# Kernel tuning notes

Hardware: AMD Instinct MI355X
Metric: run time of the kernel (lower is better)

The kernel has to match this reference:

```python
import jax, jax.numpy as jnp
import numpy as np

ALPHA = 0.2
NEG = -9e15


def _gru(x, Wih, Whh, bih, bhh):
    # x: [B, T, F]; PyTorch nn.GRU cell equations, scan over time.
    H = Whh.shape[1]
    xg = jnp.einsum('btf,gf->btg', x, Wih) + bih  # [B,T,3H]

    def step(h, gi):
        gh = h @ Whh.T + bhh
        ir, iz, inn = jnp.split(gi, 3, axis=-1)
        hr, hz, hn = jnp.split(gh, 3, axis=-1)
        r = jax.nn.sigmoid(ir + hr)
        z = jax.nn.sigmoid(iz + hz)
        n = jnp.tanh(inn + r * hn)
        h = (1.0 - z) * n + z * h
        return h, h

    h0 = jnp.zeros((x.shape[0], H), x.dtype)
    _, ys = jax.lax.scan(step, h0, jnp.swapaxes(xg, 0, 1))
    return jnp.swapaxes(ys, 0, 1)  # [B,T,H]


def _gru_attn(x, Wih, Whh, bih, bhh, aw, ab):
    out = _gru(x, Wih, Whh, bih, bhh)              # [B,T,H]
    w = jax.nn.softmax(out @ aw + ab, axis=1)       # [B,T,1]
    return jnp.sum(out * w, axis=1)                 # [B,H]


def _gat(h, mask, W, a):
    # GraphAttentionLayer with concat=True: elu(softmax(mask(leakyrelu(Wh1+Wh2^T))) @ Wh)
    Wh = h @ W                                      # [N,O]
    O = W.shape[1]
    e = jax.nn.leaky_relu((Wh @ a[:O]) + (Wh @ a[O:]).T, ALPHA)  # [N,N]
    att = jax.nn.softmax(jnp.where(mask, e, NEG), axis=1)
    return jax.nn.elu(att @ Wh)


def setup_inputs() -> dict:
    key = jax.random.key(0)
    ks = iter(jax.random.split(key, 40))
    B, S, Wk, D, F = 1, 2048, 32, 5, 16
    H, E, NS = 128, 128, 16

    def rn(shape, scale=0.1):
        return jax.random.normal(next(ks), shape, jnp.float32) * scale

    inp = {
        'stock_features': jax.random.normal(next(ks), (B, S, Wk, D, F), jnp.float32),
        'stock_to_sector': jax.random.randint(next(ks), (S,), 0, NS, jnp.int32),
        'inter_adj': jax.random.randint(next(ks), (NS, NS), 0, 2, jnp.int32),
        'gru1_Wih': rn((3 * H, F)), 'gru1_Whh': rn((3 * H, H)),
        'gru1_bih': rn((3 * H,)), 'gru1_bhh': rn((3 * H,)),
        'attn1_w': rn((H, 1)), 'attn1_b': rn((1,)),
        'gat_intra_W': rn((H, E)), 'gat_intra_a': rn((2 * E, 1)),
        'grug_Wih': rn((3 * E, E)), 'grug_Whh': rn((3 * E, E)),
        'grug_bih': rn((3 * E,)), 'grug_bhh': rn((3 * E,)),
        'attng_w': rn((E, 1)), 'attng_b': rn((1,)),
        'grua_Wih': rn((3 * E, H)), 'grua_Whh': rn((3 * E, E)),
        'grua_bih': rn((3 * E,)), 'grua_bhh': rn((3 * E,)),
        'attna_w': rn((E, 1)), 'attna_b': rn((1,)),
        'gat_inter_W': rn((E, E)), 'gat_inter_a': rn((2 * E, 1)),
        'fusion_w': rn((3 * E, E)), 'fusion_b': rn((E,)),
        'ret_w': rn((E, 1)), 'ret_b': rn((1,)),
        'mov_w': rn((E, 1)), 'mov_b': rn((1,)),
    }
    return inp


def reference(stock_features, stock_to_sector, inter_adj,
              gru1_Wih, gru1_Whh, gru1_bih, gru1_bhh, attn1_w, attn1_b,
              gat_intra_W, gat_intra_a,
              grug_Wih, grug_Whh, grug_bih, grug_bhh, attng_w, attng_b,
              grua_Wih, grua_Whh, grua_bih, grua_bhh, attna_w, attna_b,
              gat_inter_W, gat_inter_a,
              fusion_w, fusion_b, ret_w, ret_b, mov_w, mov_b):
    B, S, Wk, D, F = stock_features.shape
    H = gru1_Whh.shape[1]
    E = gat_intra_W.shape[1]
    NS = inter_adj.shape[0]

    # Short-term: GRU-attention over days, vectorized over (batch, stock, week).
    x = stock_features.reshape(B * S * Wk, D, F)
    short = _gru_attn(x, gru1_Wih, gru1_Whh, gru1_bih, gru1_bhh, attn1_w, attn1_b)
    short = short.reshape(B, S, Wk, H)

    # Intra-sector GAT on last-week embeddings; per-sector softmax == block mask.
    same_sector = stock_to_sector[:, None] == stock_to_sector[None, :]  # [S,S]
    last = short[:, :, -1, :]                                            # [B,S,H]
    intra = jax.vmap(lambda h: _gat(h, same_sector, gat_intra_W, gat_intra_a))(last)  # [B,S,E]

    # Long-term GRU-attentions.
    lg = _gru_attn(intra.reshape(B * S, 1, E), grug_Wih, grug_Whh, grug_bih, grug_bhh,
                   attng_w, attng_b).reshape(B, S, E)
    la = _gru_attn(short.reshape(B * S, Wk, H), grua_Wih, grua_Whh, grua_bih, grua_bhh,
                   attna_w, attna_b).reshape(B, S, E)

    # Sector embeddings = mean of stock long-term embeddings per sector.
    def sector_mean(g):
        sums = jax.ops.segment_sum(g, stock_to_sector, num_segments=NS)
        cnt = jax.ops.segment_sum(jnp.ones((g.shape[0], 1), g.dtype),
                                  stock_to_sector, num_segments=NS)
        return sums / jnp.maximum(cnt, 1.0)

    sec = jax.vmap(sector_mean)(lg)                                      # [B,NS,E]
    imask = inter_adj > 0
    sec_out = jax.vmap(lambda h: _gat(h, imask, gat_inter_W, gat_inter_a))(sec)
    sec_ps = sec_out[:, stock_to_sector, :]                               # [B,S,E]

    fused = jnp.concatenate([lg, la, sec_ps], axis=-1) @ fusion_w + fusion_b
    returns = (fused @ ret_w + ret_b)[..., 0]
    moves = jax.nn.sigmoid(fused @ mov_w + mov_b)[..., 0]
    return jnp.stack([returns, moves])  # [2,B,S]
```

## Files before the change

kernel.cpp:

```cpp
#include <hip/hip_runtime.h>
#include <math.h>

#define LRELU_A 0.2f
#define NEGBIG (-9.0e15f)

typedef _Float16 f16;
typedef _Float16 f16x8 __attribute__((ext_vector_type(8)));
typedef _Float16 f16x4 __attribute__((ext_vector_type(4)));
typedef float floatx4 __attribute__((ext_vector_type(4)));

__device__ __forceinline__ float rcpf(float x){ return __builtin_amdgcn_rcpf(x); }
__device__ __forceinline__ float sigm(float x){ return rcpf(1.0f+__expf(-x)); }
__device__ __forceinline__ float gru_fuse(float xr, float xz, float xn_pre, float ghn, float h){
    float Er = __expf(-xr);
    float r  = rcpf(1.0f + Er);
    float En = __expf(2.0f*(xn_pre + r*ghn));
    float Ez = __expf(-xz);
    float Dn = En + 1.0f;
    float num = fmaf(h, Dn, (En - 1.0f)*Ez);
    float den = Dn * (1.0f + Ez);
    return num * rcpf(den);
}
__device__ __forceinline__ f16x8 load_cvt8(const float* __restrict__ p){
    float4 a = *(const float4*)p; float4 b = *(const float4*)(p+4);
    f16x8 r; r[0]=(f16)a.x; r[1]=(f16)a.y; r[2]=(f16)a.z; r[3]=(f16)a.w;
    r[4]=(f16)b.x; r[5]=(f16)b.y; r[6]=(f16)b.z; r[7]=(f16)b.w;
    return r;
}
#define MFMA16(A,B,C) __builtin_amdgcn_mfma_f32_16x16x32_f16((A),(B),(C),0,0,0)

__global__ __launch_bounds__(256) void prep_kernel(
    const float* __restrict__ g1Wih, const float* __restrict__ g1Whh,
    const float* __restrict__ gaWih, const float* __restrict__ gaWhh,
    const float* __restrict__ giW,   const float* __restrict__ fw,
    const int* __restrict__ sec,
    f16* __restrict__ Wcat1, f16* __restrict__ WcatA,
    f16* __restrict__ WT, f16* __restrict__ fwT,
    int* __restrict__ memflat, int* __restrict__ pos,
    int* __restrict__ cnt, int* __restrict__ base)
{
    __shared__ int cs[16], wsc[16];
    const int b = blockIdx.x, tid = threadIdx.x;
    if (b < 160){
        for (int idx = b*256+tid; idx < 512*160; idx += 160*256){
            int r = idx/160, k = idx - r*160;
            float v = 0.0f;
            if (r < 256){ if (k < 32){ if (k < 16) v = g1Wih[r*16+k]; } else v = g1Whh[r*128 + (k-32)]; }
            else if (r < 384){ if (k < 16) v = g1Wih[r*16+k]; }
            else { if (k >= 32) v = g1Whh[(r-128)*128 + (k-32)]; }
            Wcat1[idx] = (f16)v;
        }
    } else if (b < 416){
        for (int idx = (b-160)*256+tid; idx < 512*256; idx += 256*256){
            int r = idx >> 8, k = idx & 255;
            float v = 0.0f;
            if (r < 256){ v = (k < 128) ? gaWih[r*128+k] : gaWhh[r*128 + (k-128)]; }
            else if (r < 384){ if (k < 128) v = gaWih[r*128+k]; }
            else { if (k >= 128) v = gaWhh[(r-128)*128 + (k-128)]; }
            WcatA[idx] = (f16)v;
        }
    } else if (b < 480){
        int idx = (b-416)*256+tid;
        int r = idx >> 7, c = idx & 127;
        WT[c*128 + r] = (f16)giW[idx];
    } else if (b < 672){
        int idx = (b-480)*256+tid;
        int r = idx >> 7, c = idx & 127;
        fwT[c*384 + r] = (f16)fw[idx];
    } else {
        if (tid < 16) cs[tid] = 0;
        __syncthreads();
        for (int s = tid; s < 2048; s += 256) atomicAdd(&cs[sec[s]], 1);
        __syncthreads();
        if (tid == 0){
            int acc = 0;
            for (int g=0; g<16; g++){ cnt[g]=cs[g]; base[g]=acc; wsc[g]=acc; acc+=cs[g]; }
        }
        __syncthreads();
        for (int s = tid; s < 2048; s += 256){
            int g = sec[s];
            int p = atomicAdd(&wsc[g], 1);
            memflat[p] = s;
            pos[s] = p;
        }
    }
}

__global__ __launch_bounds__(512,2) void gru_short(
    const float* __restrict__ x, const f16* __restrict__ Wcat,
    const float* __restrict__ bih, const float* __restrict__ bhh,
    const float* __restrict__ aw, const float* __restrict__ ab,
    f16* __restrict__ out)
{
    __shared__ __align__(16) f16 xs[5][32][40];
    __shared__ __align__(16) f16 hs[2][32][136];
    __shared__ float scpart[2][8][32];
    const int tid = threadIdx.x, w = tid>>6, lane = tid&63;
    const int c = lane&15, quad = lane>>4;

    { f16x4 z4 = {0,0,0,0};
      f16x4* zx = (f16x4*)&xs[0][0][0];
      for (int i=tid; i<1600; i+=512) zx[i] = z4; }

    const int jrow = w*16 + c;
    f16x8 Ar[5], Az[5], Agi, Agh[4];
#pragma unroll
    for (int kb=0;kb<5;kb++){
        Ar[kb] = *(const f16x8*)&Wcat[(size_t)(jrow)*160 + kb*32 + quad*8];
        Az[kb] = *(const f16x8*)&Wcat[(size_t)(128+jrow)*160 + kb*32 + quad*8];
    }
    Agi = *(const f16x8*)&Wcat[(size_t)(256+jrow)*160 + quad*8];
#pragma unroll
    for (int i=0;i<4;i++)
        Agh[i] = *(const f16x8*)&Wcat[(size_t)(384+jrow)*160 + 32 + i*32 + quad*8];

    float brz_r[4], brz_z[4], b_in[4], b_hn[4], awr[4];
#pragma unroll
    for (int r=0;r<4;r++){
        int j = w*16 + quad*4 + r;
        brz_r[r] = bih[j] + bhh[j];
        brz_z[r] = bih[128+j] + bhh[128+j];
        b_in[r] = bih[256+j]; b_hn[r] = bhh[256+j];
        awr[r] = aw[j];
    }
    const float abv = ab[0];

#pragma unroll 1
    for (int tile=0; tile<4; ++tile){
        const int s0 = (blockIdx.x*4 + tile)*32;
        { f16x4 z4 = {0,0,0,0};
          f16x4* zh = (f16x4*)&hs[1][0][0];
          for (int i=tid; i<1088; i+=512) zh[i] = z4; }
        for (int i=tid; i<640; i+=512){
            int s = i/20, q = i - 20*s;
            float4 v = *(const float4*)&x[(size_t)(s0+s)*80 + q*4];
            int t = (q*4)>>4, f = (q*4)&15;
            f16x4 h4; h4[0]=(f16)v.x; h4[1]=(f16)v.y; h4[2]=(f16)v.z; h4[3]=(f16)v.w;
            *(f16x4*)&xs[t][s][f] = h4;
        }
        float hreg[2][4], aacc[2][4], l_[2] = {0.0f, 0.0f};
#pragma unroll
        for (int st=0; st<2; st++)
#pragma unroll
            for (int r=0;r<4;r++){ hreg[st][r]=0.0f; aacc[st][r]=0.0f; }
        __syncthreads();

#pragma unroll 1
        for (int t=0; t<5; ++t){
            const int rp = (t&1)^1, wp = t&1;
            f16x8 Bx[2], Bh[2][4];
#pragma unroll
            for (int st=0; st<2; st++){
                Bx[st] = *(const f16x8*)&xs[t][st*16+c][quad*8];
#pragma unroll
                for (int i=0;i<4;i++)
                    Bh[st][i] = *(const f16x8*)&hs[rp][st*16+c][i*32+quad*8];
            }
            if (t > 0){
#pragma unroll
                for (int st=0; st<2; st++){
                    float sc = abv;
#pragma unroll
                    for (int ww=0; ww<8; ww++) sc += scpart[rp][ww][st*16+c];
                    float e = __expf(sc);
                    l_[st] += e;
#pragma unroll
                    for (int r=0;r<4;r++) aacc[st][r] += e*hreg[st][r];
                }
            }
            float sp[2];
#pragma unroll
            for (int st=0; st<2; st++){
                floatx4 ar = {0,0,0,0}, az = {0,0,0,0}, agi = {0,0,0,0}, agh = {0,0,0,0};
                ar = MFMA16(Ar[0], Bx[st], ar);
                az = MFMA16(Az[0], Bx[st], az);
                agi = MFMA16(Agi, Bx[st], agi);
#pragma unroll
                for (int i=0;i<4;i++){
                    ar = MFMA16(Ar[1+i], Bh[st][i], ar);
                    az = MFMA16(Az[1+i], Bh[st][i], az);
                    agh = MFMA16(Agh[i], Bh[st][i], agh);
                }
                f16x4 h4;
                sp[st] = 0.0f;
#pragma unroll
                for (int r=0;r<4;r++){
                    float hn = gru_fuse(ar[r] + brz_r[r], az[r] + brz_z[r],
                                        agi[r] + b_in[r], agh[r] + b_hn[r], hreg[st][r]);
                    hreg[st][r] = hn; h4[r] = (f16)hn;
                    sp[st] += hn * awr[r];
                }
                *(f16x4*)&hs[wp][st*16 + c][w*16 + quad*4] = h4;
            }
#pragma unroll
            for (int st=0; st<2; st++){
                sp[st] += __shfl_xor(sp[st], 16);
                sp[st] += __shfl_xor(sp[st], 32);
            }
            if (lane < 16){ scpart[wp][w][lane] = sp[0]; scpart[wp][w][16+lane] = sp[1]; }
            __syncthreads();
        }
#pragma unroll
        for (int st=0; st<2; st++){
            float sc = abv;
#pragma unroll
            for (int ww=0; ww<8; ww++) sc += scpart[0][ww][st*16+c];
            float e = __expf(sc);
            l_[st] += e;
            float inv = rcpf(l_[st]);
            f16x4 h4;
#pragma unroll
            for (int r=0;r<4;r++) h4[r] = (f16)((aacc[st][r] + e*hreg[st][r])*inv);
            *(f16x4*)&hs[0][st*16 + c][w*16 + quad*4] = h4;
        }
        __syncthreads();
        { int s = tid>>4, p = tid&15;
          *(f16x8*)&out[(size_t)(s0+s)*128 + p*8] = *(const f16x8*)&hs[0][s][p*8]; }
    }
}

__global__ __launch_bounds__(512,2) void gru_la_gatprep(
    const f16* __restrict__ xseq, const f16* __restrict__ Wcat,
    const float* __restrict__ bih, const float* __restrict__ bhh,
    const float* __restrict__ aw, const float* __restrict__ ab,
    f16* __restrict__ out,
    const f16* __restrict__ WT, const float* __restrict__ gia,
    const int* __restrict__ memflat,
    f16* __restrict__ Whs, float* __restrict__ ers, float* __restrict__ el)
{
    __shared__ __align__(16) f16 xs[2][16][136];
    __shared__ __align__(16) f16 hs[2][16][136];
    __shared__ float scpart[2][8][16];
    __shared__ __align__(16) float tbuf[32][132];
    __shared__ int rows[32];
    const int tid = threadIdx.x, w = tid>>6, lane = tid&63;
    const int c = lane&15, quad = lane>>4;

    if (blockIdx.x >= 256){
        const int p0 = (blockIdx.x-256)*32;
        if (tid < 32) rows[tid] = memflat[p0 + tid];
        __syncthreads();
        f16x8 A[2][4];
#pragma unroll
        for (int mt=0;mt<2;mt++)
#pragma unroll
            for (int kb=0;kb<4;kb++)
                A[mt][kb] = *(const f16x8*)&xseq[((size_t)rows[mt*16+c]*32 + 31)*128 + kb*32 + quad*8];
        {
            int jb = w;
            f16x8 B[4];
#pragma unroll
            for (int kb=0;kb<4;kb++)
                B[kb] = *(const f16x8*)&WT[(size_t)(jb*16+c)*128 + kb*32 + quad*8];
            floatx4 acc[2] = {{0,0,0,0},{0,0,0,0}};
#pragma unroll
            for (int kb=0;kb<4;kb++){
                acc[0] = MFMA16(A[0][kb], B[kb], acc[0]);
                acc[1] = MFMA16(A[1][kb], B[kb], acc[1]);
            }
#pragma unroll
            for (int mt=0;mt<2;mt++)
#pragma unroll
                for (int r=0;r<4;r++)
                    tbuf[mt*16 + quad*4 + r][jb*16 + c] = acc[mt][r];
        }
        __syncthreads();
        for (int i=tid; i<1024; i+=512){
            int s = i>>5, p = i&31;
            float4 v = *(const float4*)&tbuf[s][p*4];
            f16x4 h4; h4[0]=(f16)v.x; h4[1]=(f16)v.y; h4[2]=(f16)v.z; h4[3]=(f16)v.w;
            *(f16x4*)&Whs[(size_t)(p0+s)*128 + p*4] = h4;
        }
        for (int k=0; k<4; k++){
            int row = w*4 + k;
            float w0 = tbuf[row][lane], w1 = tbuf[row][64+lane];
            float v1 = w0*gia[lane]     + w1*gia[64+lane];
            float v2 = w0*gia[128+lane] + w1*gia[192+lane];
#pragma unroll
            for (int off=32; off; off>>=1){ v1 += __shfl_down(v1,off); v2 += __shfl_down(v2,off); }
            if (lane==0){ el[rows[row]] = v1; ers[p0+row] = v2; }
        }
        return;
    }
    const int s0 = blockIdx.x*8;
    { f16x4 z4 = {0,0,0,0};
      f16x4* za = (f16x4*)&xs[0][0][0];
      for (int i=tid; i<1088; i+=512) za[i] = z4;
      f16x4* zh = (f16x4*)&hs[0][0][0];
      for (int i=tid; i<1088; i+=512) zh[i] = z4; }
    __syncthreads();
    if (tid < 128){
        int s = tid>>4, p = tid&15;
        *(f16x8*)&xs[0][s][p*8] = *(const f16x8*)&xseq[((size_t)(s0+s)*32 + 0)*128 + p*8];
    }
    const int jrow = w*16 + c;
    f16x8 Ar[8], Az[8], Agi[4], Agh[4];
#pragma unroll
    for (int kb=0;kb<8;kb++){
        Ar[kb] = *(const f16x8*)&Wcat[(size_t)(jrow)*256 + kb*32 + quad*8];
        Az[kb] = *(const f16x8*)&Wcat[(size_t)(128+jrow)*256 + kb*32 + quad*8];
    }
#pragma unroll
    for (int i=0;i<4;i++){
        Agi[i] = *(const f16x8*)&Wcat[(size_t)(256+jrow)*256 + i*32 + quad*8];
        Agh[i] = *(const f16x8*)&Wcat[(size_t)(384+jrow)*256 + 128 + i*32 + quad*8];
    }
    float brz_r[4], brz_z[4], b_in[4], b_hn[4], awr[4];
#pragma unroll
    for (int r=0;r<4;r++){
        int j = w*16 + quad*4 + r;
        brz_r[r] = bih[j] + bhh[j];
        brz_z[r] = bih[128+j] + bhh[128+j];
        b_in[r] = bih[256+j]; b_hn[r] = bhh[256+j];
        awr[r] = aw[j];
    }
    const float abv = ab[0];
    float hreg[4] = {0,0,0,0}, aacc[4] = {0,0,0,0}, l_ = 0.0f;
    __syncthreads();

#pragma unroll 1
    for (int t=0; t<32; ++t){
        const int rp = (t&1)^1, wp = t&1, xp = t&1;
        f16x8 Bx[4], Bh[4];
#pragma unroll
        for (int i=0;i<4;i++){
            Bx[i] = *(const f16x8*)&xs[xp][c][i*32+quad*8];
            Bh[i] = *(const f16x8*)&hs[rp][c][i*32+quad*8];
        }
        f16x8 xstage;
        const bool do_stage = (t < 31) && (tid < 128);
        if (do_stage){
            int s = tid>>4, p = tid&15;
            xstage = *(const f16x8*)&xseq[((size_t)(s0+s)*32 + t+1)*128 + p*8];
        }
        if (t > 0){
            float sc = abv;
#pragma unroll
            for (int ww=0; ww<8; ww++) sc += scpart[rp][ww][c];
            float e = __expf(sc);
            l_ += e;
#pragma unroll
            for (int r=0;r<4;r++) aacc[r] += e*hreg[r];
        }
        floatx4 ar = {0,0,0,0}, az = {0,0,0,0}, agi = {0,0,0,0}, agh = {0,0,0,0};
#pragma unroll
        for (int i=0;i<4;i++){
            ar = MFMA16(Ar[i], Bx[i], ar);
            az = MFMA16(Az[i], Bx[i], az);
            agi = MFMA16(Agi[i], Bx[i], agi);
        }
#pragma unroll
        for (int i=0;i<4;i++){
            ar = MFMA16(Ar[4+i], Bh[i], ar);
            az = MFMA16(Az[4+i], Bh[i], az);
            agh = MFMA16(Agh[i], Bh[i], agh);
        }
        f16x4 h4;
        float sp = 0.0f;
#pragma unroll
        for (int r=0;r<4;r++){
            float hn = gru_fuse(ar[r] + brz_r[r], az[r] + brz_z[r],
                                agi[r] + b_in[r], agh[r] + b_hn[r], hreg[r]);
            hreg[r] = hn; h4[r] = (f16)hn;
            sp += hn * awr[r];
        }
        *(f16x4*)&hs[wp][c][w*16 + quad*4] = h4;
        if (do_stage){
            int s = tid>>4, p = tid&15;
            *(f16x8*)&xs[xp^1][s][p*8] = xstage;
        }
        sp += __shfl_xor(sp, 16);
        sp += __shfl_xor(sp, 32);
        if (lane < 16) scpart[wp][w][lane] = sp;
        __syncthreads();
    }
    {
        float sc = abv;
#pragma unroll
        for (int ww=0; ww<8; ww++) sc += scpart[1][ww][c];
        float e = __expf(sc);
        l_ += e;
        float inv = rcpf(l_);
        f16x4 h4;
#pragma unroll
        for (int r=0;r<4;r++) h4[r] = (f16)((aacc[r] + e*hreg[r])*inv);
        *(f16x4*)&hs[1][c][w*16 + quad*4] = h4;
    }
    __syncthreads();
    if (tid < 128){
        int s = tid>>4, p = tid&15;
        *(f16x8*)&out[(size_t)(s0+s)*128 + p*8] = *(const f16x8*)&hs[1][s][p*8];
    }
}

__global__ __launch_bounds__(256) void gat_intra_mem_kernel(
    const f16* __restrict__ Whs, const float* __restrict__ ers,
    const float* __restrict__ el, const int* __restrict__ sec,
    const int* __restrict__ cnt, const int* __restrict__ base,
    f16* __restrict__ outp, int S)
{
    int wave = threadIdx.x>>6, lane = threadIdx.x&63;
    int i = blockIdx.x*4 + wave;
    if (i>=S) return;
    int g = sec[i];
    int n = cnt[g], b = base[g];
    float eli = el[i];
    float m = -INFINITY;
    for (int jj=lane; jj<n; jj+=64){
        float v = eli + ers[b+jj]; v = v>0.f? v : LRELU_A*v;
        m = fmaxf(m, v);
    }
#pragma unroll
    for (int off=32; off; off>>=1) m = fmaxf(m, __shfl_xor(m, off));
    float l = 0.f, c0=0.f, c1=0.f;
#pragma unroll 4
    for (int jj=0; jj<n; jj++){
        float v = eli + ers[b+jj]; v = v>0.f? v : LRELU_A*v;
        float p = __expf(v-m);
        l += p;
        c0 += p*(float)Whs[(size_t)(b+jj)*128 + lane];
        c1 += p*(float)Whs[(size_t)(b+jj)*128 + 64 + lane];
    }
    float il = rcpf(l);
    c0 *= il; c1 *= il;
    outp[(size_t)i*128+lane]    = (f16)(c0>0.f? c0 : expm1f(c0));
    outp[(size_t)i*128+64+lane] = (f16)(c1>0.f? c1 : expm1f(c1));
}

__global__ __launch_bounds__(256) void lg_mfma(
    const f16* __restrict__ intra16, const float* __restrict__ Wih,
    const float* __restrict__ bih, const float* __restrict__ bhh,
    const int* __restrict__ pos,
    f16* __restrict__ lgout, f16* __restrict__ lgs)
{
    __shared__ __align__(16) f16 tbuf[32][136];
    const int tid = threadIdx.x, w = tid>>6, lane = tid&63;
    const int c = lane&15, quad = lane>>4;
    const int s0 = blockIdx.x*32;
    f16x8 A[2][4];
#pragma unroll
    for (int mt=0;mt<2;mt++)
#pragma unroll
        for (int kb=0;kb<4;kb++)
            A[mt][kb] = *(const f16x8*)&intra16[(size_t)(s0+mt*16+c)*128 + kb*32 + quad*8];
#pragma unroll
    for (int i=0;i<2;i++){
        int jb = w*2 + i;
        int j = jb*16 + c;
        f16x8 Br[4], Bz[4], Bn[4];
#pragma unroll
        for (int kb=0;kb<4;kb++){
            Br[kb] = load_cvt8(&Wih[(size_t)(j)*128 + kb*32 + quad*8]);
            Bz[kb] = load_cvt8(&Wih[(size_t)(128+j)*128 + kb*32 + quad*8]);
            Bn[kb] = load_cvt8(&Wih[(size_t)(256+j)*128 + kb*32 + quad*8]);
        }
        float b_r = bih[j] + bhh[j];
        float b_z = bih[128+j] + bhh[128+j];
        float b_i = bih[256+j], b_h = bhh[256+j];
        floatx4 ar[2] = {{0,0,0,0},{0,0,0,0}};
        floatx4 az[2] = {{0,0,0,0},{0,0,0,0}};
        floatx4 an[2] = {{0,0,0,0},{0,0,0,0}};
#pragma unroll
        for (int kb=0;kb<4;kb++)
#pragma unroll
            for (int mt=0;mt<2;mt++){
                ar[mt] = MFMA16(A[mt][kb], Br[kb], ar[mt]);
                az[mt] = MFMA16(A[mt][kb], Bz[kb], az[mt]);
                an[mt] = MFMA16(A[mt][kb], Bn[kb], an[mt]);
            }
#pragma unroll
        for (int mt=0;mt<2;mt++)
#pragma unroll
            for (int r=0;r<4;r++){
                float Er = __expf(-(ar[mt][r] + b_r));
                float rg = rcpf(1.0f + Er);
                float En = __expf(2.0f*(an[mt][r] + b_i + rg*b_h));
                float Ez = __expf(-(az[mt][r] + b_z));
                float v = (En - 1.0f)*Ez * rcpf((En + 1.0f)*(1.0f + Ez));
                tbuf[mt*16 + quad*4 + r][j] = (f16)v;
            }
    }
    __syncthreads();
    for (int i=tid; i<512; i+=256){
        int s = i>>4, p = i&15;
        f16x8 v = *(const f16x8*)&tbuf[s][p*8];
        *(f16x8*)&lgout[(size_t)(s0+s)*128 + p*8] = v;
        *(f16x8*)&lgs[(size_t)pos[s0+s]*128 + p*8] = v;
    }
}

__global__ __launch_bounds__(1024) void gat_inter_fused(
    const f16* __restrict__ lgs, const int* __restrict__ cnt,
    const int* __restrict__ base, const int* __restrict__ adj,
    const float* __restrict__ W, const float* __restrict__ a,
    float* __restrict__ outp)
{
    __shared__ __align__(16) float hs[16][132];
    __shared__ __align__(16) float Whs[16][132];
    __shared__ float el[16], er[16];
    __shared__ float att[16][16];
    const int tid = threadIdx.x, w = tid>>6, lane = tid&63;

    {
        int n = cnt[w], b = base[w];
        const int rowoff = lane>>4;
        const int colb = (lane&15)*8;
        float acc[8] = {0,0,0,0,0,0,0,0};
        for (int r = rowoff; r < n; r += 4){
            f16x8 v = *(const f16x8*)&lgs[(size_t)(b+r)*128 + colb];
#pragma unroll
            for (int k=0;k<8;k++) acc[k] += (float)v[k];
        }
#pragma unroll
        for (int k=0;k<8;k++){
            acc[k] += __shfl_xor(acc[k], 16);
            acc[k] += __shfl_xor(acc[k], 32);
        }
        if (lane < 16){
            float inv = rcpf(fmaxf((float)n, 1.0f));
#pragma unroll
            for (int k=0;k<8;k++) hs[w][colb+k] = acc[k]*inv;
        }
    }
    __syncthreads();
#pragma unroll
    for (int i=0;i<2;i++){
        int idx = i*1024 + tid; int o = idx&127, s = idx>>7;
        float a0=0.f,a1=0.f,a2=0.f,a3=0.f;
        for (int j=0;j<128;j+=4){
            a0 += hs[s][j]  *W[(j  )*128+o];
            a1 += hs[s][j+1]*W[(j+1)*128+o];
            a2 += hs[s][j+2]*W[(j+2)*128+o];
            a3 += hs[s][j+3]*W[(j+3)*128+o];
        }
        Whs[s][o]=(a0+a1)+(a2+a3);
    }
    __syncthreads();
    {
        int half = lane>>5, l = lane&31;
        const float* av = a + half*128;
        float acc2 = 0.f;
#pragma unroll
        for (int k=0;k<4;k++) acc2 += Whs[w][l+32*k]*av[l+32*k];
#pragma unroll
        for (int off=1; off<32; off<<=1) acc2 += __shfl_xor(acc2, off);
        if (l==0){ if (half) er[w]=acc2; else el[w]=acc2; }
    }
    __syncthreads();
    if (tid<16){
        int i=tid; float m=NEGBIG; float e[16];
        for(int j=0;j<16;j++){
            float v = el[i]+er[j]; v = v>0.f? v : LRELU_A*v;
            e[j] = (adj[i*16+j]>0)? v : NEGBIG;
            m = fmaxf(m,e[j]);
        }
        float l=0.f;
        for(int j=0;j<16;j++){ float p=__expf(e[j]-m); att[i][j]=p; l+=p; }
        float il = rcpf(l);
        for(int j=0;j<16;j++) att[i][j] *= il;
    }
    __syncthreads();
#pragma unroll
    for (int i=0;i<2;i++){
        int idx=i*1024+tid; int o=idx&127, s=idx>>7;
        float acc=0.f;
#pragma unroll
        for(int j=0;j<16;j++) acc += att[s][j]*Whs[j][o];
        outp[s*128+o] = acc>0.f? acc : expm1f(acc);
    }
}

__global__ __launch_bounds__(256) void fused_mfma(
    const f16* __restrict__ lg16, const f16* __restrict__ la16,
    const float* __restrict__ seco, const int* __restrict__ sec,
    const f16* __restrict__ fwT,
    const float* __restrict__ fb, const float* __restrict__ rw,
    const float* __restrict__ rb, const float* __restrict__ mw,
    const float* __restrict__ mb, float* __restrict__ outp)
{
    __shared__ float rpart[4][32], mpart[4][32];
    const int tid = threadIdx.x, w = tid>>6, lane = tid&63;
    const int c = lane&15, quad = lane>>4;
    const int s0 = blockIdx.x*32;
    f16x8 A[2][12];
#pragma unroll
    for (int mt=0;mt<2;mt++){
        int row = s0 + mt*16 + c;
        int g = sec[row];
#pragma unroll
        for (int kb=0;kb<4;kb++){
            A[mt][kb]   = *(const f16x8*)&lg16[(size_t)row*128 + kb*32 + quad*8];
            A[mt][4+kb] = *(const f16x8*)&la16[(size_t)row*128 + kb*32 + quad*8];
            A[mt][8+kb] = load_cvt8(&seco[(size_t)g*128 + kb*32 + quad*8]);
        }
    }
    float rsum[2][4] = {{0,0,0,0},{0,0,0,0}};
    float msum[2][4] = {{0,0,0,0},{0,0,0,0}};
#pragma unroll
    for (int i=0;i<2;i++){
        int jb = w*2 + i;
        int col = jb*16 + c;
        f16x8 B[12];
#pragma unroll
        for (int kb=0;kb<12;kb++)
            B[kb] = *(const f16x8*)&fwT[(size_t)col*384 + kb*32 + quad*8];
        floatx4 acc[2] = {{0,0,0,0},{0,0,0,0}};
#pragma unroll
        for (int kb=0;kb<12;kb++){
            acc[0] = MFMA16(A[0][kb], B[kb], acc[0]);
            acc[1] = MFMA16(A[1][kb], B[kb], acc[1]);
        }
        float fbv = fb[col], rwv = rw[col], mwv = mw[col];
#pragma unroll
        for (int mt=0;mt<2;mt++)
#pragma unroll
            for (int r=0;r<4;r++){
                float fu = acc[mt][r] + fbv;
                rsum[mt][r] += fu*rwv;
                msum[mt][r] += fu*mwv;
            }
    }
#pragma unroll
    for (int mt=0;mt<2;mt++)
#pragma unroll
        for (int r=0;r<4;r++){
#pragma unroll
            for (int off=1; off<16; off<<=1){
                rsum[mt][r] += __shfl_xor(rsum[mt][r], off);
                msum[mt][r] += __shfl_xor(msum[mt][r], off);
            }
            if (c==0){
                rpart[w][mt*16 + quad*4 + r] = rsum[mt][r];
                mpart[w][mt*16 + quad*4 + r] = msum[mt][r];
            }
        }
    __syncthreads();
    if (tid < 32){
        int s = tid;
        float rs = rb[0], ms = mb[0];
#pragma unroll
        for (int ww=0; ww<4; ww++){ rs += rpart[ww][s]; ms += mpart[ww][s]; }
        outp[s0+s] = rs;
        outp[2048 + s0 + s] = sigm(ms);
    }
}

extern "C" void kernel_launch(void* const* d_in, const int* in_sizes, int n_in,
                              void* d_out, int out_size, void* d_ws, size_t ws_size,
                              hipStream_t stream) {
    const float* sf    = (const float*)d_in[0];
    const int*   sec   = (const int*)  d_in[1];
    const int*   adj   = (const int*)  d_in[2];
    const float* g1Wih = (const float*)d_in[3];
    const float* g1Whh = (const float*)d_in[4];
    const float* g1bih = (const float*)d_in[5];
    const float* g1bhh = (const float*)d_in[6];
    const float* a1w   = (const float*)d_in[7];
    const float* a1b   = (const float*)d_in[8];
    const float* giW   = (const float*)d_in[9];
    const float* gia   = (const float*)d_in[10];
    const float* ggWih = (const float*)d_in[11];
    const float* ggbih = (const float*)d_in[13];
    const float* ggbhh = (const float*)d_in[14];
    const float* gaWih = (const float*)d_in[17];
    const float* gaWhh = (const float*)d_in[18];
    const float* gabih = (const float*)d_in[19];
    const float* gabhh = (const float*)d_in[20];
    const float* aaw   = (const float*)d_in[21];
    const float* aab   = (const float*)d_in[22];
    const float* geW   = (const float*)d_in[23];
    const float* gea   = (const float*)d_in[24];
    const float* fw    = (const float*)d_in[25];
    const float* fb    = (const float*)d_in[26];
    const float* rw    = (const float*)d_in[27];
    const float* rb    = (const float*)d_in[28];
    const float* mw    = (const float*)d_in[29];
    const float* mb    = (const float*)d_in[30];

    char* p = (char*)d_ws;
    f16*   shrt16 = (f16*)p;   p += (size_t)65536*128*2;
    f16*   intra16= (f16*)p;   p += (size_t)262144*2;
    f16*   lg16   = (f16*)p;   p += (size_t)262144*2;
    f16*   la16   = (f16*)p;   p += (size_t)262144*2;
    f16*   Whs    = (f16*)p;   p += (size_t)262144*2;
    f16*   lgs    = (f16*)p;   p += (size_t)262144*2;
    f16*   Wcat1  = (f16*)p;   p += (size_t)512*160*2;
    f16*   WcatA  = (f16*)p;   p += (size_t)512*256*2;
    f16*   WT     = (f16*)p;   p += (size_t)16384*2;
    f16*   fwT    = (f16*)p;   p += (size_t)49152*2;
    float* el     = (float*)p; p += 2048*4;
    float* ers    = (float*)p; p += 2048*4;
    float* seco   = (float*)p; p += 2048*4;
    int*   memflat= (int*)p;   p += 2048*4;
    int*   pos    = (int*)p;   p += 2048*4;
    int*   cnt    = (int*)p;   p += 16*4;
    int*   basep  = (int*)p;   p += 16*4;

    prep_kernel<<<673,256,0,stream>>>(g1Wih, g1Whh, gaWih, gaWhh, giW, fw, sec,
                                      Wcat1, WcatA, WT, fwT, memflat, pos, cnt, basep);
    gru_short<<<512,512,0,stream>>>(sf, Wcat1, g1bih, g1bhh, a1w, a1b, shrt16);
    gru_la_gatprep<<<320,512,0,stream>>>(shrt16, WcatA, gabih, gabhh, aaw, aab, la16,
                                         WT, gia, memflat, Whs, ers, el);
    gat_intra_mem_kernel<<<512,256,0,stream>>>(Whs, ers, el, sec, cnt, basep, intra16, 2048);
    lg_mfma<<<64,256,0,stream>>>(intra16, ggWih, ggbih, ggbhh, pos, lg16, lgs);
    gat_inter_fused<<<1,1024,0,stream>>>(lgs, cnt, basep, adj, geW, gea, seco);
    fused_mfma<<<64,256,0,stream>>>(lg16, la16, seco, sec, fwT, fb, rw, rb, mw, mb, (float*)d_out);
}
```

Before: 306.5 us.

## Prefetch GRU input tiles, halve gru_short grid, use MFMA for inter-sector GAT projection

gru_short now processes 8 tiles per block instead of 4, running on half as many blocks, and prefetches the next tile's input features into registers while the current tile's recurrence runs. This hides global load latency behind compute. Separately, the single-block inter-sector GAT replaces its scalar fp32 128x128 projection with f16 MFMA, using a transposed f16 weight copy built in the prep kernel. The MFMA path lowers precision in that layer, and the smaller grid may leave compute units underused on a 256-CU part.

```diff
diff --git a/kernel.cpp b/kernel.cpp
--- a/kernel.cpp
+++ b/kernel.cpp
@@ -33,9 +33,10 @@
     const float* __restrict__ g1Wih, const float* __restrict__ g1Whh,
     const float* __restrict__ gaWih, const float* __restrict__ gaWhh,
     const float* __restrict__ giW,   const float* __restrict__ fw,
+    const float* __restrict__ geW,
     const int* __restrict__ sec,
     f16* __restrict__ Wcat1, f16* __restrict__ WcatA,
-    f16* __restrict__ WT, f16* __restrict__ fwT,
+    f16* __restrict__ WT, f16* __restrict__ fwT, f16* __restrict__ geWT,
     int* __restrict__ memflat, int* __restrict__ pos,
     int* __restrict__ cnt, int* __restrict__ base)
 {
@@ -67,6 +68,10 @@
         int idx = (b-480)*256+tid;
         int r = idx >> 7, c = idx & 127;
         fwT[c*384 + r] = (f16)fw[idx];
+    } else if (b < 736){
+        int idx = (b-672)*256+tid;
+        int r = idx >> 7, c = idx & 127;
+        geWT[c*128 + r] = (f16)geW[idx];
     } else {
         if (tid < 16) cs[tid] = 0;
         __syncthreads();
@@ -125,18 +130,37 @@
     }
     const float abv = ab[0];
 
+    const int s0i = tid/20,        q0 = tid - 20*s0i;
+    const int i1  = tid + 512;
+    const int s1i = i1/20,         q1 = i1 - 20*s1i;
+    const bool pf1 = (tid < 128);
+    float4 xpf0, xpf1;
+    {
+        const size_t base0 = (size_t)(blockIdx.x*8)*32;
+        xpf0 = *(const float4*)&x[(base0 + s0i)*80 + q0*4];
+        if (pf1) xpf1 = *(const float4*)&x[(base0 + s1i)*80 + q1*4];
+    }
+
 #pragma unroll 1
-    for (int tile=0; tile<4; ++tile){
-        const int s0 = (blockIdx.x*4 + tile)*32;
+    for (int tile=0; tile<8; ++tile){
+        const int s0 = (blockIdx.x*8 + tile)*32;
         { f16x4 z4 = {0,0,0,0};
           f16x4* zh = (f16x4*)&hs[1][0][0];
           for (int i=tid; i<1088; i+=512) zh[i] = z4; }
-        for (int i=tid; i<640; i+=512){
-            int s = i/20, q = i - 20*s;
-            float4 v = *(const float4*)&x[(size_t)(s0+s)*80 + q*4];
-            int t = (q*4)>>4, f = (q*4)&15;
-            f16x4 h4; h4[0]=(f16)v.x; h4[1]=(f16)v.y; h4[2]=(f16)v.z; h4[3]=(f16)v.w;
-            *(f16x4*)&xs[t][s][f] = h4;
+        {
+            int t = (q0*4)>>4, f = (q0*4)&15;
+            f16x4 h4; h4[0]=(f16)xpf0.x; h4[1]=(f16)xpf0.y; h4[2]=(f16)xpf0.z; h4[3]=(f16)xpf0.w;
+            *(f16x4*)&xs[t][s0i][f] = h4;
+            if (pf1){
+                int t1 = (q1*4)>>4, f1 = (q1*4)&15;
+                f16x4 g4; g4[0]=(f16)xpf1.x; g4[1]=(f16)xpf1.y; g4[2]=(f16)xpf1.z; g4[3]=(f16)xpf1.w;
+                *(f16x4*)&xs[t1][s1i][f1] = g4;
+            }
+        }
+        if (tile < 7){
+            const size_t basen = (size_t)(s0 + 32);
+            xpf0 = *(const float4*)&x[(basen + s0i)*80 + q0*4];
+            if (pf1) xpf1 = *(const float4*)&x[(basen + s1i)*80 + q1*4];
         }
         float hreg[2][4], aacc[2][4], l_[2] = {0.0f, 0.0f};
 #pragma unroll
@@ -492,7 +516,7 @@
 __global__ __launch_bounds__(1024) void gat_inter_fused(
     const f16* __restrict__ lgs, const int* __restrict__ cnt,
     const int* __restrict__ base, const int* __restrict__ adj,
-    const float* __restrict__ W, const float* __restrict__ a,
+    const f16* __restrict__ geWT, const float* __restrict__ a,
     float* __restrict__ outp)
 {
     __shared__ __align__(16) float hs[16][132];
@@ -500,6 +524,7 @@
     __shared__ float el[16], er[16];
     __shared__ float att[16][16];
     const int tid = threadIdx.x, w = tid>>6, lane = tid&63;
+    const int c = lane&15, quad = lane>>4;
 
     {
         int n = cnt[w], b = base[w];
@@ -523,17 +548,18 @@
         }
     }
     __syncthreads();
-#pragma unroll
-    for (int i=0;i<2;i++){
-        int idx = i*1024 + tid; int o = idx&127, s = idx>>7;
-        float a0=0.f,a1=0.f,a2=0.f,a3=0.f;
-        for (int j=0;j<128;j+=4){
-            a0 += hs[s][j]  *W[(j  )*128+o];
-            a1 += hs[s][j+1]*W[(j+1)*128+o];
-            a2 += hs[s][j+2]*W[(j+2)*128+o];
-            a3 += hs[s][j+3]*W[(j+3)*128+o];
-        }
-        Whs[s][o]=(a0+a1)+(a2+a3);
+    if (w < 8){
+        f16x8 A[4], B[4];
+#pragma unroll
+        for (int kb=0;kb<4;kb++){
+            A[kb] = load_cvt8(&hs[c][kb*32 + quad*8]);
+            B[kb] = *(const f16x8*)&geWT[(size_t)(w*16+c)*128 + kb*32 + quad*8];
+        }
+        floatx4 acc = {0,0,0,0};
+#pragma unroll
+        for (int kb=0;kb<4;kb++) acc = MFMA16(A[kb], B[kb], acc);
+#pragma unroll
+        for (int r=0;r<4;r++) Whs[quad*4 + r][w*16 + c] = acc[r];
     }
     __syncthreads();
     {
@@ -687,6 +713,7 @@
     f16*   Wcat1  = (f16*)p;   p += (size_t)512*160*2;
     f16*   WcatA  = (f16*)p;   p += (size_t)512*256*2;
     f16*   WT     = (f16*)p;   p += (size_t)16384*2;
+    f16*   geWT   = (f16*)p;   p += (size_t)16384*2;
     f16*   fwT    = (f16*)p;   p += (size_t)49152*2;
     float* el     = (float*)p; p += 2048*4;
     float* ers    = (float*)p; p += 2048*4;
@@ -696,13 +723,13 @@
     int*   cnt    = (int*)p;   p += 16*4;
     int*   basep  = (int*)p;   p += 16*4;
 
-    prep_kernel<<<673,256,0,stream>>>(g1Wih, g1Whh, gaWih, gaWhh, giW, fw, sec,
-                                      Wcat1, WcatA, WT, fwT, memflat, pos, cnt, basep);
-    gru_short<<<512,512,0,stream>>>(sf, Wcat1, g1bih, g1bhh, a1w, a1b, shrt16);
+    prep_kernel<<<737,256,0,stream>>>(g1Wih, g1Whh, gaWih, gaWhh, giW, fw, geW, sec,
+                                      Wcat1, WcatA, WT, fwT, geWT, memflat, pos, cnt, basep);
+    gru_short<<<256,512,0,stream>>>(sf, Wcat1, g1bih, g1bhh, a1w, a1b, shrt16);
     gru_la_gatprep<<<320,512,0,stream>>>(shrt16, WcatA, gabih, gabhh, aaw, aab, la16,
                                          WT, gia, memflat, Whs, ers, el);
     gat_intra_mem_kernel<<<512,256,0,stream>>>(Whs, ers, el, sec, cnt, basep, intra16, 2048);
     lg_mfma<<<64,256,0,stream>>>(intra16, ggWih, ggbih, ggbhh, pos, lg16, lgs);
-    gat_inter_fused<<<1,1024,0,stream>>>(lgs, cnt, basep, adj, geW, gea, seco);
+    gat_inter_fused<<<1,1024,0,stream>>>(lgs, cnt, basep, adj, geWT, gea, seco);
     fused_mfma<<<64,256,0,stream>>>(lg16, la16, seco, sec, fwT, fb, rw, rb, mw, mb, (float*)d_out);
 }
```

After: 299.0 us. 2.4% less time.
